# Kernel tuning notes

Measured on AMD Instinct MI355X. Metric: run time of the kernel, lower is better.

Reference implementation:

```python
import jax, jax.numpy as jnp
import numpy as np

N, K = 8192, 32
DIM_INP_Q, DIM_INP_KV, DIM, DIM_OUT = 256, 256, 256, 512


def setup_inputs() -> dict:
    key = jax.random.key(0)
    ks = jax.random.split(key, 16)
    s = lambda k_, shp: jax.random.normal(k_, shp, dtype=jnp.float32) * 0.05
    return {
        "xyz_q": jax.random.normal(ks[0], (N, 3), dtype=jnp.float32),
        "feats_q": jax.random.normal(ks[1], (N, DIM_INP_Q), dtype=jnp.float32),
        "xyz_kv": jax.random.normal(ks[2], (N, K, 3), dtype=jnp.float32),
        "feats_kv": jax.random.normal(ks[3], (N, K, DIM_INP_KV), dtype=jnp.float32),
        # linear weights stored (in, out); y = x @ W + b
        "Wq": s(ks[4], (DIM_INP_Q, DIM)),
        "Wk": s(ks[5], (DIM_INP_KV, DIM)),
        "Wv": s(ks[6], (DIM_INP_KV, DIM)),
        "d1_w": s(ks[7], (3, DIM // 2)), "d1_b": jnp.zeros((DIM // 2,), jnp.float32),
        "d2_w": s(ks[8], (DIM // 2, DIM)), "d2_b": jnp.zeros((DIM,), jnp.float32),
        "g1_w": s(ks[9], (DIM, DIM)), "g1_b": jnp.zeros((DIM,), jnp.float32),
        "g2_w": s(ks[10], (DIM, DIM)), "g2_b": jnp.zeros((DIM,), jnp.float32),
        "out_w": s(ks[11], (DIM, DIM_OUT)), "out_b": jnp.zeros((DIM_OUT,), jnp.float32),
    }


def reference(xyz_q, feats_q, xyz_kv, feats_kv, Wq, Wk, Wv,
              d1_w, d1_b, d2_w, d2_b, g1_w, g1_b, g2_w, g2_b, out_w, out_b):
    q_attn = feats_q @ Wq                      # (N, dim)
    k_attn = feats_kv @ Wk                     # (N, k, dim)
    v_attn = feats_kv @ Wv                     # (N, k, dim)
    # relative-position MLP: (N, k, 3) -> (N, k, dim)
    rel = xyz_q[:, None, :] - xyz_kv
    pos_encode = jax.nn.relu(rel @ d1_w + d1_b) @ d2_w + d2_b
    # subtractive vector attention scores through fc_gamma MLP
    h = q_attn[:, None, :] - k_attn + pos_encode
    attn = jax.nn.relu(h @ g1_w + g1_b) @ g2_w + g2_b   # (N, k, dim)
    attn = jax.nn.softmax(attn, axis=-2)                # softmax over neighbors k
    res = jnp.einsum('nmf,nmf->nf', attn, v_attn + pos_encode)
    res = res @ out_w + out_b                           # (N, dim_out)
    return (xyz_q, res)
```

## Files before the change

kernel.cpp:

```cpp
#include <hip/hip_runtime.h>
#include <hip/hip_bf16.h>

#define NPTS 8192
#define KN   32
#define DIM  256
#define DH   128
#define DOUT 512

typedef __attribute__((ext_vector_type(8))) short bf16x8;
typedef __attribute__((ext_vector_type(4))) short short4v;
typedef __attribute__((ext_vector_type(4))) float f32x4;

#define MFMA16(a, b, c) __builtin_amdgcn_mfma_f32_16x16x32_bf16((a), (b), (c), 0, 0, 0)

__device__ __forceinline__ short f2b(float f) {
    __hip_bfloat16 h = __float2bfloat16(f);
    return *reinterpret_cast<short*>(&h);
}

#define WSO_QATTN 0u
#define WSO_RES   8388608u
#define WSO_WKT   16777216u
#define WSO_WVT   16908288u
#define WSO_G1T   17039360u
#define WSO_G2T   17170432u
#define WSO_D2T   17301504u
#define WSO_OWT   17367040u

extern "C" __global__ __launch_bounds__(256)
void prep_w(const float* __restrict__ Wk, const float* __restrict__ Wv,
            const float* __restrict__ g1w, const float* __restrict__ g2w,
            const float* __restrict__ d2w, const float* __restrict__ ow,
            short* __restrict__ wkT, short* __restrict__ wvT,
            short* __restrict__ g1T, short* __restrict__ g2T,
            short* __restrict__ d2T, short* __restrict__ owT)
{
    const int idx = blockIdx.x * 256 + threadIdx.x;
    if (idx < 65536) {
        const int o = idx >> 8, i = idx & 255;
        wkT[idx] = f2b(-Wk[i * 256 + o]);
        wvT[idx] = f2b(Wv[i * 256 + o]);
        g1T[idx] = f2b(g1w[i * 256 + o]);
        g2T[idx] = f2b(g2w[i * 256 + o]);
    }
    if (idx < 32768) {
        const int o = idx >> 7, i = idx & 127;
        d2T[idx] = f2b(d2w[i * 256 + o]);
    }
    if (idx < 131072) {
        const int o = idx >> 8, i = idx & 255;
        owT[idx] = f2b(ow[i * 512 + o]);
    }
}

extern "C" __global__ __launch_bounds__(256)
void prep_q(const float* __restrict__ feats_q, const float* __restrict__ Wq,
            const float* __restrict__ xyz_q, float* __restrict__ q_attn,
            float* __restrict__ out)
{
    const int b = blockIdx.x;
    const int t = threadIdx.x;
    if (b >= 512) {
        const int idx = (b - 512) * 256 + t;
        out[idx] = xyz_q[idx];
        return;
    }
    __shared__ float s_q[16][256];
    for (int j = 0; j < 16; ++j)
        s_q[j][t] = feats_q[(size_t)(b * 16 + j) * 256 + t];
    __syncthreads();
    float acc[16];
    #pragma unroll
    for (int pt = 0; pt < 16; ++pt) acc[pt] = 0.f;
    for (int k = 0; k < 256; ++k) {
        const float wv = Wq[k * 256 + t];
        #pragma unroll
        for (int pt = 0; pt < 16; ++pt) acc[pt] = fmaf(s_q[pt][k], wv, acc[pt]);
    }
    #pragma unroll
    for (int pt = 0; pt < 16; ++pt)
        q_attn[(size_t)(b * 16 + pt) * 256 + t] = acc[pt];
}


#define STAGE_FEATS(koff)                                                         \
    {                                                                             \
        const float* fp_ = feats_kv + ((size_t)p0 * KN + srow) * DIM + (koff) +   \
                           scs * 32;                                              \
        _Pragma("unroll")                                                         \
        for (int j_ = 0; j_ < 8; ++j_) {                                          \
            const float4 v_ = *(const float4*)(fp_ + 4 * j_);                     \
            const int c2_ = scs * 32 + 4 * j_;                                    \
            short4v t_;                                                           \
            t_[0] = f2b(v_.x); t_[1] = f2b(v_.y);                                 \
            t_[2] = f2b(v_.z); t_[3] = f2b(v_.w);                                 \
            *(short4v*)&s_lds[srow * 128 + (c2_ ^ ((srow & 7) << 3))] = t_;       \
        }                                                                         \
    }

extern "C" __global__ __launch_bounds__(512, 2)
void ctb_main(const float* __restrict__ xyz_q, const float* __restrict__ xyz_kv,
              const float* __restrict__ feats_kv,
              const float* __restrict__ d1w, const float* __restrict__ d1b,
              const float* __restrict__ d2b, const float* __restrict__ g1b,
              const float* __restrict__ g2b,
              const float* __restrict__ q_attn,
              const short* __restrict__ wkTn, const short* __restrict__ wvT,
              const short* __restrict__ g1T, const short* __restrict__ g2T,
              const short* __restrict__ d2T,
              float* __restrict__ res_ws)
{
    extern __shared__ short s_lds[];
    const int t    = threadIdx.x;
    const int w    = t >> 6;
    const int lane = t & 63;
    const int q    = lane >> 4;
    const int ln   = lane & 15;
    const int p0   = blockIdx.x * 4;
    const int colbase = 32 * w + ln;

    const int srow = t >> 2;
    const int scs  = t & 3;

    STAGE_FEATS(0);
    {
        const int pt = srow >> 5;
        const float qx = xyz_q[(p0 + pt) * 3 + 0];
        const float qy = xyz_q[(p0 + pt) * 3 + 1];
        const float qz = xyz_q[(p0 + pt) * 3 + 2];
        const float* xk = xyz_kv + ((size_t)p0 * KN + srow) * 3;
        const float rx = qx - xk[0], ry = qy - xk[1], rz = qz - xk[2];
        #pragma unroll
        for (int j = 0; j < 32; ++j) {
            const int c = scs * 32 + j;
            const float v = fmaxf(fmaf(rx, d1w[c],
                                  fmaf(ry, d1w[DH + c],
                                  fmaf(rz, d1w[2 * DH + c], d1b[c]))), 0.f);
            s_lds[16384 + srow * 128 + (c ^ ((srow & 7) << 3))] = f2b(v);
        }
    }
    __syncthreads();

    f32x4 vp[8][2];
    #pragma unroll
    for (int nt = 0; nt < 2; ++nt) {
        const float bb = d2b[colbase + 16 * nt];
        #pragma unroll
        for (int mt = 0; mt < 8; ++mt) vp[mt][nt] = (f32x4){bb, bb, bb, bb};
    }
    #pragma unroll
    for (int ks = 0; ks < 4; ++ks) {
        bf16x8 ar[8];
        #pragma unroll
        for (int mt = 0; mt < 8; ++mt) {
            const int row = 16 * mt + ln;
            ar[mt] = *(const bf16x8*)&s_lds[16384 + row * 128 +
                                            ((32 * ks + 8 * q) ^ ((row & 7) << 3))];
        }
        #pragma unroll
        for (int nt = 0; nt < 2; ++nt) {
            const bf16x8 bb = *(const bf16x8*)(d2T + (colbase + 16 * nt) * DH +
                                               32 * ks + 8 * q);
            #pragma unroll
            for (int mt = 0; mt < 8; ++mt)
                vp[mt][nt] = MFMA16(ar[mt], bb, vp[mt][nt]);
        }
    }
    f32x4 hacc[8][2];
    #pragma unroll
    for (int nt = 0; nt < 2; ++nt)
        #pragma unroll
        for (int pt = 0; pt < 4; ++pt) {
            const float qv = q_attn[(size_t)(p0 + pt) * DIM + colbase + 16 * nt];
            #pragma unroll
            for (int m2 = 0; m2 < 2; ++m2) {
                const int mt = 2 * pt + m2;
                #pragma unroll
                for (int r = 0; r < 4; ++r) hacc[mt][nt][r] = vp[mt][nt][r] + qv;
            }
        }
    #pragma unroll
    for (int half = 0; half < 2; ++half) {
        if (half) {
            __syncthreads();
            STAGE_FEATS(128);
            __syncthreads();
        }
        #pragma unroll
        for (int ksl = 0; ksl < 4; ++ksl) {
            const int ks = 4 * half + ksl;
            bf16x8 af[8];
            #pragma unroll
            for (int mt = 0; mt < 8; ++mt) {
                const int row = 16 * mt + ln;
                af[mt] = *(const bf16x8*)&s_lds[row * 128 +
                                                ((32 * ksl + 8 * q) ^ ((row & 7) << 3))];
            }
            #pragma unroll
            for (int nt = 0; nt < 2; ++nt) {
                const int co = (colbase + 16 * nt) * DIM + 32 * ks + 8 * q;
                const bf16x8 bk = *(const bf16x8*)(wkTn + co);
                const bf16x8 bv = *(const bf16x8*)(wvT + co);
                #pragma unroll
                for (int mt = 0; mt < 8; ++mt) {
                    hacc[mt][nt] = MFMA16(af[mt], bk, hacc[mt][nt]);
                    vp[mt][nt]   = MFMA16(af[mt], bv, vp[mt][nt]);
                }
            }
        }
    }
    __syncthreads();
    #pragma unroll
    for (int mt = 0; mt < 8; ++mt)
        #pragma unroll
        for (int nt = 0; nt < 2; ++nt)
            #pragma unroll
            for (int r = 0; r < 4; ++r) {
                const int row = 16 * mt + 4 * q + r;
                const int col = colbase + 16 * nt;
                s_lds[row * 256 + (col ^ ((row & 7) << 3))] = f2b(hacc[mt][nt][r]);
            }
    __syncthreads();

    {
        f32x4 tacc[8][2];
        #pragma unroll
        for (int nt = 0; nt < 2; ++nt) {
            const float bb = g1b[colbase + 16 * nt];
            #pragma unroll
            for (int mt = 0; mt < 8; ++mt) tacc[mt][nt] = (f32x4){bb, bb, bb, bb};
        }
        #pragma unroll
        for (int ks = 0; ks < 8; ++ks) {
            bf16x8 ah[8];
            #pragma unroll
            for (int mt = 0; mt < 8; ++mt) {
                const int row = 16 * mt + ln;
                ah[mt] = *(const bf16x8*)&s_lds[row * 256 +
                                                ((32 * ks + 8 * q) ^ ((row & 7) << 3))];
            }
            #pragma unroll
            for (int nt = 0; nt < 2; ++nt) {
                const bf16x8 bb = *(const bf16x8*)(g1T + (colbase + 16 * nt) * DIM +
                                                   32 * ks + 8 * q);
                #pragma unroll
                for (int mt = 0; mt < 8; ++mt)
                    tacc[mt][nt] = MFMA16(ah[mt], bb, tacc[mt][nt]);
            }
        }
        __syncthreads();
        #pragma unroll
        for (int mt = 0; mt < 8; ++mt)
            #pragma unroll
            for (int nt = 0; nt < 2; ++nt)
                #pragma unroll
                for (int r = 0; r < 4; ++r) {
                    const int row = 16 * mt + 4 * q + r;
                    const int col = colbase + 16 * nt;
                    s_lds[row * 256 + (col ^ ((row & 7) << 3))] =
                        f2b(fmaxf(tacc[mt][nt][r], 0.f));
                }
        __syncthreads();
    }

    {
        f32x4 ap[8][2];
        #pragma unroll
        for (int nt = 0; nt < 2; ++nt) {
            const float bb = g2b[colbase + 16 * nt];
            #pragma unroll
            for (int mt = 0; mt < 8; ++mt) ap[mt][nt] = (f32x4){bb, bb, bb, bb};
        }
        #pragma unroll
        for (int ks = 0; ks < 8; ++ks) {
            bf16x8 at[8];
            #pragma unroll
            for (int mt = 0; mt < 8; ++mt) {
                const int row = 16 * mt + ln;
                at[mt] = *(const bf16x8*)&s_lds[row * 256 +
                                                ((32 * ks + 8 * q) ^ ((row & 7) << 3))];
            }
            #pragma unroll
            for (int nt = 0; nt < 2; ++nt) {
                const bf16x8 bb = *(const bf16x8*)(g2T + (colbase + 16 * nt) * DIM +
                                                   32 * ks + 8 * q);
                #pragma unroll
                for (int mt = 0; mt < 8; ++mt)
                    ap[mt][nt] = MFMA16(at[mt], bb, ap[mt][nt]);
            }
        }

        float stot[4][2];
        #pragma unroll
        for (int pt = 0; pt < 4; ++pt)
            #pragma unroll
            for (int nt = 0; nt < 2; ++nt) {
                float m = -1e30f;
                #pragma unroll
                for (int m2 = 0; m2 < 2; ++m2)
                    #pragma unroll
                    for (int r = 0; r < 4; ++r)
                        m = fmaxf(m, ap[2 * pt + m2][nt][r]);
                m = fmaxf(m, __shfl_xor(m, 16, 64));
                m = fmaxf(m, __shfl_xor(m, 32, 64));
                float s = 0.f;
                #pragma unroll
                for (int m2 = 0; m2 < 2; ++m2)
                    #pragma unroll
                    for (int r = 0; r < 4; ++r) {
                        const float e = __expf(ap[2 * pt + m2][nt][r] - m);
                        ap[2 * pt + m2][nt][r] = e;
                        s += e;
                    }
                s += __shfl_xor(s, 16, 64);
                s += __shfl_xor(s, 32, 64);
                stot[pt][nt] = s;
            }

        #pragma unroll
        for (int pt = 0; pt < 4; ++pt)
            #pragma unroll
            for (int nt = 0; nt < 2; ++nt) {
                float racc = 0.f;
                #pragma unroll
                for (int m2 = 0; m2 < 2; ++m2)
                    #pragma unroll
                    for (int r = 0; r < 4; ++r)
                        racc = fmaf(ap[2 * pt + m2][nt][r], vp[2 * pt + m2][nt][r],
                                    racc);
                racc += __shfl_xor(racc, 16, 64);
                racc += __shfl_xor(racc, 32, 64);
                if (q == 0)
                    res_ws[(size_t)(p0 + pt) * DIM + colbase + 16 * nt] =
                        racc / stot[pt][nt];
            }
    }
}

extern "C" __global__ __launch_bounds__(256, 2)
void ctb_out(const float* __restrict__ res_ws, const short* __restrict__ owT,
             const float* __restrict__ ob, float* __restrict__ out)
{
    __shared__ __align__(16) short s_a[64 * 256];
    const int t = threadIdx.x, w = t >> 6, lane = t & 63, q = lane >> 4, ln = lane & 15;
    const int rowbase = blockIdx.x * 64;

    {
        const int row = t >> 2;
        const int cs  = t & 3;
        const float* src = res_ws + (size_t)(rowbase + row) * DIM + cs * 64;
        #pragma unroll
        for (int j = 0; j < 16; ++j) {
            const float4 v = *(const float4*)(src + 4 * j);
            const int c = cs * 64 + 4 * j;
            short4v sv;
            sv[0] = f2b(v.x); sv[1] = f2b(v.y); sv[2] = f2b(v.z); sv[3] = f2b(v.w);
            *(short4v*)&s_a[row * 256 + (c ^ ((row & 7) << 3))] = sv;
        }
    }
    __syncthreads();

    const int colbase = 128 * w + ln;
    f32x4 acc[4][8];
    #pragma unroll
    for (int nt = 0; nt < 8; ++nt) {
        const float bb = ob[colbase + 16 * nt];
        #pragma unroll
        for (int mt = 0; mt < 4; ++mt) acc[mt][nt] = (f32x4){bb, bb, bb, bb};
    }
    #pragma unroll
    for (int ks = 0; ks < 8; ++ks) {
        bf16x8 af[4];
        #pragma unroll
        for (int mt = 0; mt < 4; ++mt) {
            const int row = 16 * mt + ln;
            af[mt] = *(const bf16x8*)&s_a[row * 256 +
                                          ((32 * ks + 8 * q) ^ ((row & 7) << 3))];
        }
        #pragma unroll
        for (int nt = 0; nt < 8; ++nt) {
            const bf16x8 bb = *(const bf16x8*)(owT + (colbase + 16 * nt) * DIM +
                                               32 * ks + 8 * q);
            #pragma unroll
            for (int mt = 0; mt < 4; ++mt)
                acc[mt][nt] = MFMA16(af[mt], bb, acc[mt][nt]);
        }
    }
    float* o = out + (size_t)NPTS * 3;
    #pragma unroll
    for (int mt = 0; mt < 4; ++mt)
        #pragma unroll
        for (int nt = 0; nt < 8; ++nt)
            #pragma unroll
            for (int r = 0; r < 4; ++r) {
                const int row = 16 * mt + 4 * q + r;
                const int col = colbase + 16 * nt;
                o[(size_t)(rowbase + row) * DOUT + col] = acc[mt][nt][r];
            }
}

extern "C" void kernel_launch(void* const* d_in, const int* in_sizes, int n_in,
                              void* d_out, int out_size, void* d_ws, size_t ws_size,
                              hipStream_t stream) {
    const float* xyz_q    = (const float*)d_in[0];
    const float* feats_q  = (const float*)d_in[1];
    const float* xyz_kv   = (const float*)d_in[2];
    const float* feats_kv = (const float*)d_in[3];
    const float* Wq       = (const float*)d_in[4];
    const float* Wk       = (const float*)d_in[5];
    const float* Wv       = (const float*)d_in[6];
    const float* d1w      = (const float*)d_in[7];
    const float* d1b      = (const float*)d_in[8];
    const float* d2w      = (const float*)d_in[9];
    const float* d2b      = (const float*)d_in[10];
    const float* g1w      = (const float*)d_in[11];
    const float* g1b      = (const float*)d_in[12];
    const float* g2w      = (const float*)d_in[13];
    const float* g2b      = (const float*)d_in[14];
    const float* ow       = (const float*)d_in[15];
    const float* ob       = (const float*)d_in[16];
    float* out = (float*)d_out;

    char* ws = (char*)d_ws;
    float* q_attn = (float*)(ws + WSO_QATTN);
    float* res_ws = (float*)(ws + WSO_RES);
    short* wkT    = (short*)(ws + WSO_WKT);
    short* wvT    = (short*)(ws + WSO_WVT);
    short* g1T    = (short*)(ws + WSO_G1T);
    short* g2T    = (short*)(ws + WSO_G2T);
    short* d2T    = (short*)(ws + WSO_D2T);
    short* owT    = (short*)(ws + WSO_OWT);

    prep_w<<<dim3(512), dim3(256), 0, stream>>>(Wk, Wv, g1w, g2w, d2w, ow,
                                                wkT, wvT, g1T, g2T, d2T, owT);
    prep_q<<<dim3(608), dim3(256), 0, stream>>>(feats_q, Wq, xyz_q, q_attn, out);
    ctb_main<<<dim3(2048), dim3(512), 65536, stream>>>(
        xyz_q, xyz_kv, feats_kv, d1w, d1b, d2b, g1b, g2b,
        q_attn, wkT, wvT, g1T, g2T, d2T, res_ws);
    ctb_out<<<dim3(128), dim3(256), 0, stream>>>(res_ws, owT, ob, out);
}
```

Baseline: 677.4 us.

## Halve points per block in main kernel, raise occupancy, retile prep and output kernels

The main kernel now processes 2 points (64 rows) per block instead of 4. It stages the full 256-wide feats_kv tile at once instead of in two halves, and uses 48KB of LDS with a minimum of 4 blocks per SM. Register tiles shrink accordingly, which is meant to raise occupancy and remove a mid-loop sync and restage. The weight transpose now goes through LDS tiles for coalesced access, prep_q handles 32 rows per block with vectorized LDS reads, and ctb_out uses 32-row tiles with padded LDS and preloaded A fragments. The trade-off is that each block reuses its weight-fragment loads over fewer rows, so L2 traffic for the weights roughly doubles.

Result: slower. 785.6 us (+16.0%).

```diff
diff --git a/kernel.cpp b/kernel.cpp
--- a/kernel.cpp
+++ b/kernel.cpp
@@ -35,21 +35,42 @@
             short* __restrict__ g1T, short* __restrict__ g2T,
             short* __restrict__ d2T, short* __restrict__ owT)
 {
-    const int idx = blockIdx.x * 256 + threadIdx.x;
-    if (idx < 65536) {
-        const int o = idx >> 8, i = idx & 255;
-        wkT[idx] = f2b(-Wk[i * 256 + o]);
-        wvT[idx] = f2b(Wv[i * 256 + o]);
-        g1T[idx] = f2b(g1w[i * 256 + o]);
-        g2T[idx] = f2b(g2w[i * 256 + o]);
-    }
-    if (idx < 32768) {
-        const int o = idx >> 7, i = idx & 127;
-        d2T[idx] = f2b(d2w[i * 256 + o]);
-    }
-    if (idx < 131072) {
-        const int o = idx >> 8, i = idx & 255;
-        owT[idx] = f2b(ow[i * 512 + o]);
+    __shared__ float s_t[64][65];
+    const int bid = blockIdx.x, t = threadIdx.x;
+    const float* src; short* dst;
+    int scols, dcols, O, I;
+    bool neg = false;
+    if (bid < 64) {
+        const int mat = bid >> 4, tile = bid & 15;
+        O = (tile >> 2) * 64; I = (tile & 3) * 64;
+        scols = 256; dcols = 256;
+        if (mat == 0)      { src = Wk;  dst = wkT; neg = true; }
+        else if (mat == 1) { src = Wv;  dst = wvT; }
+        else if (mat == 2) { src = g1w; dst = g1T; }
+        else               { src = g2w; dst = g2T; }
+    } else if (bid < 72) {
+        const int tile = bid - 64;
+        O = (tile >> 1) * 64; I = (tile & 1) * 64;
+        src = d2w; dst = d2T; scols = 256; dcols = 128;
+    } else {
+        const int tile = bid - 72;
+        O = (tile >> 2) * 64; I = (tile & 3) * 64;
+        src = ow; dst = owT; scols = 512; dcols = 256;
+    }
+    #pragma unroll
+    for (int rep = 0; rep < 16; ++rep) {
+        const int lin = rep * 256 + t;
+        s_t[lin >> 6][lin & 63] =
+            src[(size_t)(I + (lin >> 6)) * scols + O + (lin & 63)];
+    }
+    __syncthreads();
+    #pragma unroll
+    for (int rep = 0; rep < 16; ++rep) {
+        const int lin = rep * 256 + t;
+        const int o = lin >> 6, i = lin & 63;
+        float v = s_t[i][o];
+        if (neg) v = -v;
+        dst[(size_t)(O + o) * dcols + I + i] = f2b(v);
     }
 }
 
@@ -60,45 +81,38 @@
 {
     const int b = blockIdx.x;
     const int t = threadIdx.x;
-    if (b >= 512) {
-        const int idx = (b - 512) * 256 + t;
+    if (b >= 256) {
+        const int idx = (b - 256) * 256 + t;
         out[idx] = xyz_q[idx];
         return;
     }
-    __shared__ float s_q[16][256];
-    for (int j = 0; j < 16; ++j)
-        s_q[j][t] = feats_q[(size_t)(b * 16 + j) * 256 + t];
-    __syncthreads();
-    float acc[16];
-    #pragma unroll
-    for (int pt = 0; pt < 16; ++pt) acc[pt] = 0.f;
-    for (int k = 0; k < 256; ++k) {
-        const float wv = Wq[k * 256 + t];
-        #pragma unroll
-        for (int pt = 0; pt < 16; ++pt) acc[pt] = fmaf(s_q[pt][k], wv, acc[pt]);
-    }
-    #pragma unroll
-    for (int pt = 0; pt < 16; ++pt)
-        q_attn[(size_t)(b * 16 + pt) * 256 + t] = acc[pt];
-}
-
-
-#define STAGE_FEATS(koff)                                                         \
-    {                                                                             \
-        const float* fp_ = feats_kv + ((size_t)p0 * KN + srow) * DIM + (koff) +   \
-                           scs * 32;                                              \
-        _Pragma("unroll")                                                         \
-        for (int j_ = 0; j_ < 8; ++j_) {                                          \
-            const float4 v_ = *(const float4*)(fp_ + 4 * j_);                     \
-            const int c2_ = scs * 32 + 4 * j_;                                    \
-            short4v t_;                                                           \
-            t_[0] = f2b(v_.x); t_[1] = f2b(v_.y);                                 \
-            t_[2] = f2b(v_.z); t_[3] = f2b(v_.w);                                 \
-            *(short4v*)&s_lds[srow * 128 + (c2_ ^ ((srow & 7) << 3))] = t_;       \
-        }                                                                         \
-    }
-
-extern "C" __global__ __launch_bounds__(512, 2)
+    __shared__ float s_q[32][256];
+    for (int j = 0; j < 32; ++j)
+        s_q[j][t] = feats_q[(size_t)(b * 32 + j) * 256 + t];
+    __syncthreads();
+    float acc[32];
+    #pragma unroll
+    for (int pt = 0; pt < 32; ++pt) acc[pt] = 0.f;
+    for (int k = 0; k < 256; k += 4) {
+        float wv0 = Wq[(k + 0) * 256 + t];
+        float wv1 = Wq[(k + 1) * 256 + t];
+        float wv2 = Wq[(k + 2) * 256 + t];
+        float wv3 = Wq[(k + 3) * 256 + t];
+        #pragma unroll
+        for (int pt = 0; pt < 32; ++pt) {
+            const float4 sv = *(const float4*)&s_q[pt][k];
+            acc[pt] = fmaf(sv.x, wv0, acc[pt]);
+            acc[pt] = fmaf(sv.y, wv1, acc[pt]);
+            acc[pt] = fmaf(sv.z, wv2, acc[pt]);
+            acc[pt] = fmaf(sv.w, wv3, acc[pt]);
+        }
+    }
+    #pragma unroll
+    for (int pt = 0; pt < 32; ++pt)
+        q_attn[(size_t)(b * 32 + pt) * 256 + t] = acc[pt];
+}
+
+extern "C" __global__ __launch_bounds__(512, 4)
 void ctb_main(const float* __restrict__ xyz_q, const float* __restrict__ xyz_kv,
               const float* __restrict__ feats_kv,
               const float* __restrict__ d1w, const float* __restrict__ d1b,
@@ -116,14 +130,21 @@
     const int lane = t & 63;
     const int q    = lane >> 4;
     const int ln   = lane & 15;
-    const int p0   = blockIdx.x * 4;
+    const int p0   = blockIdx.x * 2;
     const int colbase = 32 * w + ln;
 
-    const int srow = t >> 2;
-    const int scs  = t & 3;
-
-    STAGE_FEATS(0);
     {
+        const int srow = t >> 3;
+        const int sc   = t & 7;
+        const float* fp = feats_kv + ((size_t)p0 * KN + srow) * DIM + sc * 32;
+        #pragma unroll
+        for (int j = 0; j < 8; ++j) {
+            const float4 v = *(const float4*)(fp + 4 * j);
+            const int c = sc * 32 + 4 * j;
+            short4v sv;
+            sv[0] = f2b(v.x); sv[1] = f2b(v.y); sv[2] = f2b(v.z); sv[3] = f2b(v.w);
+            *(short4v*)&s_lds[srow * 256 + (c ^ ((srow & 7) << 3))] = sv;
+        }
         const int pt = srow >> 5;
         const float qx = xyz_q[(p0 + pt) * 3 + 0];
         const float qy = xyz_q[(p0 + pt) * 3 + 1];
@@ -131,8 +152,8 @@
         const float* xk = xyz_kv + ((size_t)p0 * KN + srow) * 3;
         const float rx = qx - xk[0], ry = qy - xk[1], rz = qz - xk[2];
         #pragma unroll
-        for (int j = 0; j < 32; ++j) {
-            const int c = scs * 32 + j;
+        for (int j = 0; j < 16; ++j) {
+            const int c = sc * 16 + j;
             const float v = fmaxf(fmaf(rx, d1w[c],
                                   fmaf(ry, d1w[DH + c],
                                   fmaf(rz, d1w[2 * DH + c], d1b[c]))), 0.f);
@@ -141,18 +162,18 @@
     }
     __syncthreads();
 
-    f32x4 vp[8][2];
+    f32x4 vp[4][2];
     #pragma unroll
     for (int nt = 0; nt < 2; ++nt) {
         const float bb = d2b[colbase + 16 * nt];
         #pragma unroll
-        for (int mt = 0; mt < 8; ++mt) vp[mt][nt] = (f32x4){bb, bb, bb, bb};
+        for (int mt = 0; mt < 4; ++mt) vp[mt][nt] = (f32x4){bb, bb, bb, bb};
     }
     #pragma unroll
     for (int ks = 0; ks < 4; ++ks) {
-        bf16x8 ar[8];
-        #pragma unroll
-        for (int mt = 0; mt < 8; ++mt) {
+        bf16x8 ar[4];
+        #pragma unroll
+        for (int mt = 0; mt < 4; ++mt) {
             const int row = 16 * mt + ln;
             ar[mt] = *(const bf16x8*)&s_lds[16384 + row * 128 +
                                             ((32 * ks + 8 * q) ^ ((row & 7) << 3))];
@@ -162,56 +183,49 @@
             const bf16x8 bb = *(const bf16x8*)(d2T + (colbase + 16 * nt) * DH +
                                                32 * ks + 8 * q);
             #pragma unroll
-            for (int mt = 0; mt < 8; ++mt)
-                vp[mt][nt] = MFMA16(ar[mt], bb, vp[mt][nt]);
-        }
-    }
-    f32x4 hacc[8][2];
-    #pragma unroll
-    for (int nt = 0; nt < 2; ++nt)
-        #pragma unroll
-        for (int pt = 0; pt < 4; ++pt) {
-            const float qv = q_attn[(size_t)(p0 + pt) * DIM + colbase + 16 * nt];
-            #pragma unroll
-            for (int m2 = 0; m2 < 2; ++m2) {
-                const int mt = 2 * pt + m2;
-                #pragma unroll
-                for (int r = 0; r < 4; ++r) hacc[mt][nt][r] = vp[mt][nt][r] + qv;
-            }
-        }
-    #pragma unroll
-    for (int half = 0; half < 2; ++half) {
-        if (half) {
-            __syncthreads();
-            STAGE_FEATS(128);
-            __syncthreads();
-        }
-        #pragma unroll
-        for (int ksl = 0; ksl < 4; ++ksl) {
-            const int ks = 4 * half + ksl;
-            bf16x8 af[8];
-            #pragma unroll
-            for (int mt = 0; mt < 8; ++mt) {
-                const int row = 16 * mt + ln;
-                af[mt] = *(const bf16x8*)&s_lds[row * 128 +
-                                                ((32 * ksl + 8 * q) ^ ((row & 7) << 3))];
-            }
-            #pragma unroll
-            for (int nt = 0; nt < 2; ++nt) {
-                const int co = (colbase + 16 * nt) * DIM + 32 * ks + 8 * q;
-                const bf16x8 bk = *(const bf16x8*)(wkTn + co);
-                const bf16x8 bv = *(const bf16x8*)(wvT + co);
-                #pragma unroll
-                for (int mt = 0; mt < 8; ++mt) {
-                    hacc[mt][nt] = MFMA16(af[mt], bk, hacc[mt][nt]);
-                    vp[mt][nt]   = MFMA16(af[mt], bv, vp[mt][nt]);
-                }
-            }
-        }
-    }
-    __syncthreads();
-    #pragma unroll
-    for (int mt = 0; mt < 8; ++mt)
+            for (int mt = 0; mt < 4; ++mt) vp[mt][nt] = MFMA16(ar[mt], bb, vp[mt][nt]);
+        }
+    }
+    f32x4 hacc[4][2];
+    {
+        float qv[2][2];
+        #pragma unroll
+        for (int pt = 0; pt < 2; ++pt)
+            #pragma unroll
+            for (int nt = 0; nt < 2; ++nt)
+                qv[pt][nt] = q_attn[(size_t)(p0 + pt) * DIM + colbase + 16 * nt];
+        #pragma unroll
+        for (int mt = 0; mt < 4; ++mt)
+            #pragma unroll
+            for (int nt = 0; nt < 2; ++nt)
+                #pragma unroll
+                for (int r = 0; r < 4; ++r)
+                    hacc[mt][nt][r] = vp[mt][nt][r] + qv[mt >> 1][nt];
+    }
+    #pragma unroll
+    for (int ks = 0; ks < 8; ++ks) {
+        bf16x8 af[4];
+        #pragma unroll
+        for (int mt = 0; mt < 4; ++mt) {
+            const int row = 16 * mt + ln;
+            af[mt] = *(const bf16x8*)&s_lds[row * 256 +
+                                            ((32 * ks + 8 * q) ^ ((row & 7) << 3))];
+        }
+        #pragma unroll
+        for (int nt = 0; nt < 2; ++nt) {
+            const int co = (colbase + 16 * nt) * DIM + 32 * ks + 8 * q;
+            const bf16x8 bk = *(const bf16x8*)(wkTn + co);
+            const bf16x8 bv = *(const bf16x8*)(wvT + co);
+            #pragma unroll
+            for (int mt = 0; mt < 4; ++mt) {
+                hacc[mt][nt] = MFMA16(af[mt], bk, hacc[mt][nt]);
+                vp[mt][nt]   = MFMA16(af[mt], bv, vp[mt][nt]);
+            }
+        }
+    }
+    __syncthreads();
+    #pragma unroll
+    for (int mt = 0; mt < 4; ++mt)
         #pragma unroll
         for (int nt = 0; nt < 2; ++nt)
             #pragma unroll
@@ -223,18 +237,18 @@
     __syncthreads();
 
     {
-        f32x4 tacc[8][2];
+        f32x4 tacc[4][2];
         #pragma unroll
         for (int nt = 0; nt < 2; ++nt) {
             const float bb = g1b[colbase + 16 * nt];
             #pragma unroll
-            for (int mt = 0; mt < 8; ++mt) tacc[mt][nt] = (f32x4){bb, bb, bb, bb};
+            for (int mt = 0; mt < 4; ++mt) tacc[mt][nt] = (f32x4){bb, bb, bb, bb};
         }
         #pragma unroll
         for (int ks = 0; ks < 8; ++ks) {
-            bf16x8 ah[8];
-            #pragma unroll
-            for (int mt = 0; mt < 8; ++mt) {
+            bf16x8 ah[4];
+            #pragma unroll
+            for (int mt = 0; mt < 4; ++mt) {
                 const int row = 16 * mt + ln;
                 ah[mt] = *(const bf16x8*)&s_lds[row * 256 +
                                                 ((32 * ks + 8 * q) ^ ((row & 7) << 3))];
@@ -244,13 +258,13 @@
                 const bf16x8 bb = *(const bf16x8*)(g1T + (colbase + 16 * nt) * DIM +
                                                    32 * ks + 8 * q);
                 #pragma unroll
-                for (int mt = 0; mt < 8; ++mt)
+                for (int mt = 0; mt < 4; ++mt)
                     tacc[mt][nt] = MFMA16(ah[mt], bb, tacc[mt][nt]);
             }
         }
         __syncthreads();
         #pragma unroll
-        for (int mt = 0; mt < 8; ++mt)
+        for (int mt = 0; mt < 4; ++mt)
             #pragma unroll
             for (int nt = 0; nt < 2; ++nt)
                 #pragma unroll
@@ -264,18 +278,18 @@
     }
 
     {
-        f32x4 ap[8][2];
+        f32x4 ap[4][2];
         #pragma unroll
         for (int nt = 0; nt < 2; ++nt) {
             const float bb = g2b[colbase + 16 * nt];
             #pragma unroll
-            for (int mt = 0; mt < 8; ++mt) ap[mt][nt] = (f32x4){bb, bb, bb, bb};
+            for (int mt = 0; mt < 4; ++mt) ap[mt][nt] = (f32x4){bb, bb, bb, bb};
         }
         #pragma unroll
         for (int ks = 0; ks < 8; ++ks) {
-            bf16x8 at[8];
-            #pragma unroll
-            for (int mt = 0; mt < 8; ++mt) {
+            bf16x8 at[4];
+            #pragma unroll
+            for (int mt = 0; mt < 4; ++mt) {
                 const int row = 16 * mt + ln;
                 at[mt] = *(const bf16x8*)&s_lds[row * 256 +
                                                 ((32 * ks + 8 * q) ^ ((row & 7) << 3))];
@@ -285,14 +299,13 @@
                 const bf16x8 bb = *(const bf16x8*)(g2T + (colbase + 16 * nt) * DIM +
                                                    32 * ks + 8 * q);
                 #pragma unroll
-                for (int mt = 0; mt < 8; ++mt)
+                for (int mt = 0; mt < 4; ++mt)
                     ap[mt][nt] = MFMA16(at[mt], bb, ap[mt][nt]);
             }
         }
 
-        float stot[4][2];
-        #pragma unroll
-        for (int pt = 0; pt < 4; ++pt)
+        #pragma unroll
+        for (int pt = 0; pt < 2; ++pt)
             #pragma unroll
             for (int nt = 0; nt < 2; ++nt) {
                 float m = -1e30f;
@@ -314,13 +327,6 @@
                     }
                 s += __shfl_xor(s, 16, 64);
                 s += __shfl_xor(s, 32, 64);
-                stot[pt][nt] = s;
-            }
-
-        #pragma unroll
-        for (int pt = 0; pt < 4; ++pt)
-            #pragma unroll
-            for (int nt = 0; nt < 2; ++nt) {
                 float racc = 0.f;
                 #pragma unroll
                 for (int m2 = 0; m2 < 2; ++m2)
@@ -331,8 +337,7 @@
                 racc += __shfl_xor(racc, 16, 64);
                 racc += __shfl_xor(racc, 32, 64);
                 if (q == 0)
-                    res_ws[(size_t)(p0 + pt) * DIM + colbase + 16 * nt] =
-                        racc / stot[pt][nt];
+                    res_ws[(size_t)(p0 + pt) * DIM + colbase + 16 * nt] = racc / s;
             }
     }
 }
@@ -341,54 +346,54 @@
 void ctb_out(const float* __restrict__ res_ws, const short* __restrict__ owT,
              const float* __restrict__ ob, float* __restrict__ out)
 {
-    __shared__ __align__(16) short s_a[64 * 256];
+    __shared__ __align__(16) short s_a[32][264];
     const int t = threadIdx.x, w = t >> 6, lane = t & 63, q = lane >> 4, ln = lane & 15;
-    const int rowbase = blockIdx.x * 64;
+    const int rowbase = blockIdx.x * 32;
 
     {
-        const int row = t >> 2;
-        const int cs  = t & 3;
-        const float* src = res_ws + (size_t)(rowbase + row) * DIM + cs * 64;
-        #pragma unroll
-        for (int j = 0; j < 16; ++j) {
-            const float4 v = *(const float4*)(src + 4 * j);
-            const int c = cs * 64 + 4 * j;
-            short4v sv;
-            sv[0] = f2b(v.x); sv[1] = f2b(v.y); sv[2] = f2b(v.z); sv[3] = f2b(v.w);
-            *(short4v*)&s_a[row * 256 + (c ^ ((row & 7) << 3))] = sv;
-        }
-    }
-    __syncthreads();
+        const int row = t >> 3;
+        const int c0  = (t & 7) * 32;
+        const float* src = res_ws + (size_t)(rowbase + row) * DIM + c0;
+        #pragma unroll
+        for (int j = 0; j < 32; j += 4) {
+            const float4 v = *(const float4*)(src + j);
+            s_a[row][c0 + j + 0] = f2b(v.x);
+            s_a[row][c0 + j + 1] = f2b(v.y);
+            s_a[row][c0 + j + 2] = f2b(v.z);
+            s_a[row][c0 + j + 3] = f2b(v.w);
+        }
+    }
+    __syncthreads();
+
+    bf16x8 af[2][8];
+    #pragma unroll
+    for (int mt = 0; mt < 2; ++mt)
+        #pragma unroll
+        for (int ks = 0; ks < 8; ++ks)
+            af[mt][ks] = *(const bf16x8*)&s_a[16 * mt + ln][32 * ks + 8 * q];
 
     const int colbase = 128 * w + ln;
-    f32x4 acc[4][8];
+    f32x4 acc[2][8];
     #pragma unroll
     for (int nt = 0; nt < 8; ++nt) {
         const float bb = ob[colbase + 16 * nt];
         #pragma unroll
-        for (int mt = 0; mt < 4; ++mt) acc[mt][nt] = (f32x4){bb, bb, bb, bb};
+        for (int mt = 0; mt < 2; ++mt) acc[mt][nt] = (f32x4){bb, bb, bb, bb};
     }
     #pragma unroll
     for (int ks = 0; ks < 8; ++ks) {
-        bf16x8 af[4];
-        #pragma unroll
-        for (int mt = 0; mt < 4; ++mt) {
-            const int row = 16 * mt + ln;
-            af[mt] = *(const bf16x8*)&s_a[row * 256 +
-                                          ((32 * ks + 8 * q) ^ ((row & 7) << 3))];
-        }
+        const short* bp = owT + 32 * ks + 8 * q;
         #pragma unroll
         for (int nt = 0; nt < 8; ++nt) {
-            const bf16x8 bb = *(const bf16x8*)(owT + (colbase + 16 * nt) * DIM +
-                                               32 * ks + 8 * q);
-            #pragma unroll
-            for (int mt = 0; mt < 4; ++mt)
-                acc[mt][nt] = MFMA16(af[mt], bb, acc[mt][nt]);
+            const bf16x8 bb = *(const bf16x8*)(bp + (colbase + 16 * nt) * DIM);
+            #pragma unroll
+            for (int mt = 0; mt < 2; ++mt)
+                acc[mt][nt] = MFMA16(af[mt][ks], bb, acc[mt][nt]);
         }
     }
     float* o = out + (size_t)NPTS * 3;
     #pragma unroll
-    for (int mt = 0; mt < 4; ++mt)
+    for (int mt = 0; mt < 2; ++mt)
         #pragma unroll
         for (int nt = 0; nt < 8; ++nt)
             #pragma unroll
@@ -431,11 +436,11 @@
     short* d2T    = (short*)(ws + WSO_D2T);
     short* owT    = (short*)(ws + WSO_OWT);
 
-    prep_w<<<dim3(512), dim3(256), 0, stream>>>(Wk, Wv, g1w, g2w, d2w, ow,
+    prep_w<<<dim3(104), dim3(256), 0, stream>>>(Wk, Wv, g1w, g2w, d2w, ow,
                                                 wkT, wvT, g1T, g2T, d2T, owT);
-    prep_q<<<dim3(608), dim3(256), 0, stream>>>(feats_q, Wq, xyz_q, q_attn, out);
-    ctb_main<<<dim3(2048), dim3(512), 65536, stream>>>(
+    prep_q<<<dim3(352), dim3(256), 0, stream>>>(feats_q, Wq, xyz_q, q_attn, out);
+    ctb_main<<<dim3(4096), dim3(512), 49152, stream>>>(
         xyz_q, xyz_kv, feats_kv, d1w, d1b, d2b, g1b, g2b,
         q_attn, wkT, wvT, g1T, g2T, d2T, res_ws);
-    ctb_out<<<dim3(128), dim3(256), 0, stream>>>(res_ws, owT, ob, out);
-}
+    ctb_out<<<dim3(256), dim3(256), 0, stream>>>(res_ws, owT, ob, out);
+}
```
